# Optimization experiments

Hardware: AMD Instinct MI355X
Metric: run time of the kernel (lower is better)

## Reference

```python
import jax, jax.numpy as jnp
import numpy as np


def _gru_cell(x, h, W_ih, W_hh, b_ih, b_hh):
    # torch.nn.GRUCell semantics, gate order (r, z, n)
    gi = x @ W_ih.T + b_ih          # [B, 3H]
    gh = h @ W_hh.T + b_hh          # [B, 3H]
    ir, iz, inn = jnp.split(gi, 3, axis=-1)
    hr, hz, hn = jnp.split(gh, 3, axis=-1)
    r = jax.nn.sigmoid(ir + hr)
    z = jax.nn.sigmoid(iz + hz)
    n = jnp.tanh(inn + r * hn)
    return (1.0 - z) * n + z * h


def setup_inputs() -> dict:
    key = jax.random.key(0)
    ks = jax.random.split(key, 9)
    B, T, X, H = 128, 512, 64, 256
    s = 0.05
    return {
        "input": jax.random.normal(ks[0], (B, T, X), jnp.float32),
        "h_enc": jax.random.normal(ks[1], (B, H), jnp.float32),
        "W_ih": jax.random.normal(ks[2], (3 * H, X), jnp.float32) * s,
        "W_hh": jax.random.normal(ks[3], (3 * H, H), jnp.float32) * s,
        "b_ih": jnp.zeros((3 * H,), jnp.float32),
        "b_hh": jnp.zeros((3 * H,), jnp.float32),
        "W_out": jax.random.normal(ks[4], (X, H), jnp.float32) * s,
        "b_out": jnp.zeros((X,), jnp.float32),
        "mask0": jax.random.randint(ks[5], (T,), 0, 2, jnp.int32),
        "mask1": jax.random.randint(ks[6], (T,), 0, 2, jnp.int32),
        "skip_size": 4,
    }


def _skip_tables(T, skip):
    # Replicates Python-list negative indexing of the original forward.
    # Skip-list position at the GRU call (pre-append):  2i   if i<skip else i-skip
    # Skip-list position at the projection (post-append): 2i+1 if i<skip else i-skip
    # Positions < skip are zero placeholders; position p >= skip is H[p-skip].
    g_idx = np.zeros(T, np.int32); g_zero = np.zeros(T, bool)
    p_idx = np.zeros(T, np.int32); p_zero = np.zeros(T, bool)
    for i in range(T):
        pg = 2 * i if i < skip else i - skip
        pp = 2 * i + 1 if i < skip else i - skip
        g_zero[i] = pg < skip; g_idx[i] = max(pg - skip, 0)
        p_zero[i] = pp < skip; p_idx[i] = max(pp - skip, 0)
    return g_idx, g_zero, p_idx, p_zero


def reference(input, h_enc, W_ih, W_hh, b_ih, b_hh, W_out, b_out, mask0, mask1, skip_size):
    B, T, X = input.shape
    H = h_enc.shape[1]
    g_idx, g_zero, p_idx, p_zero = _skip_tables(T, int(skip_size))
    m0 = mask0.astype(input.dtype)
    m1 = mask1.astype(input.dtype)

    xs = (jnp.arange(T), m0, m1,
          jnp.asarray(g_idx), jnp.asarray(g_zero),
          jnp.asarray(p_idx), jnp.asarray(p_zero))

    def step(carry, sx):
        h_prev, x_prev, buf = carry          # buf: [T, B, H] history of GRU outputs
        i, a0, a1, gi, gz, pi, pz = sx
        skip_g = jnp.where(gz, 0.0, buf[gi])            # [B, H]
        hidden = h_prev * a0 + skip_g * a1
        h_new = _gru_cell(x_prev, hidden, W_ih, W_hh, b_ih, b_hh)
        buf = buf.at[i].set(h_new)                       # append H[i]
        skip_p = jnp.where(pz, 0.0, buf[pi])
        out = (h_prev + skip_p) @ W_out.T + b_out        # [B, X]
        return (h_new, out, buf), out

    buf0 = jnp.zeros((T, B, H), input.dtype)
    go = jnp.zeros((B, X), input.dtype)                  # GO token
    (_, _, _), outs = jax.lax.scan(step, (h_enc, go, buf0), xs)
    return jnp.transpose(outs, (1, 0, 2))                # [B, T, X]
```

## Files before the change

kernel.cpp:

```cpp
#include <hip/hip_runtime.h>

typedef _Float16 h2_t __attribute__((ext_vector_type(2)));

constexpr int T_ = 512;
constexpr int X_ = 64;
constexpr int H_ = 256;
constexpr int NWG = 128;
constexpr int NT = 512;
constexpr int RS = 16;

constexpr int GHH_U4 = 3 * 2 * 16 * 256;
constexpr int GIH_U4 = 3 * 2 * 4 * 256;
constexpr int GOUT_U4 = 2048;
constexpr int G_TOTAL = GHH_U4 + GIH_U4 + GOUT_U4;

__device__ __forceinline__ float sigmoid_f(float x) {
  float e = __expf(fminf(-x, 80.f));
  return 1.f / (1.f + e);
}
__device__ __forceinline__ float tanh_f(float x) {
  float e = __expf(fminf(-2.f * x, 80.f));
  return (1.f - e) / (1.f + e);
}

__device__ __forceinline__ unsigned pk2(float a, float b) {
  h2_t v;
  v[0] = (_Float16)a;
  v[1] = (_Float16)b;
  return __builtin_bit_cast(unsigned, v);
}
__device__ __forceinline__ uint4 pk8(const float* s) {
  return make_uint4(pk2(s[0], s[1]), pk2(s[2], s[3]), pk2(s[4], s[5]),
                    pk2(s[6], s[7]));
}

__device__ __forceinline__ float dotp(unsigned w, unsigned h, float acc) {
  h2_t wv = __builtin_bit_cast(h2_t, w);
  h2_t hv = __builtin_bit_cast(h2_t, h);
#if __has_builtin(__builtin_amdgcn_fdot2)
  return __builtin_amdgcn_fdot2(wv, hv, acc, false);
#else
  acc = fmaf((float)wv[0], (float)hv[0], acc);
  return fmaf((float)wv[1], (float)hv[1], acc);
#endif
}
__device__ __forceinline__ float dotq(uint4 w, uint4 h, float acc) {
  acc = dotp(w.x, h.x, acc);
  acc = dotp(w.y, h.y, acc);
  acc = dotp(w.z, h.z, acc);
  acc = dotp(w.w, h.w, acc);
  return acc;
}

__global__ void prep_kernel(const float* __restrict__ Wih,
                            const float* __restrict__ Whh,
                            const float* __restrict__ Wout,
                            uint4* __restrict__ G) {
  int id = blockIdx.x * 256 + threadIdx.x;
  if (id < GHH_U4) {
    int c = id & 255, r = id >> 8;
    int j = r & 15, gk = r >> 4, g = gk >> 1, kh = gk & 1;
    G[id] = pk8(Whh + (size_t)(g * 256 + c) * H_ + kh * 128 + j * 8);
  } else if (id < GHH_U4 + GIH_U4) {
    int jd = id - GHH_U4;
    int c = jd & 255, r = jd >> 8;
    int j = r & 3, gk = r >> 2, g = gk >> 1, kh = gk & 1;
    G[id] = pk8(Wih + (size_t)(g * 256 + c) * X_ + kh * 32 + j * 8);
  } else if (id < G_TOTAL) {
    int jd = id - GHH_U4 - GIH_U4;
    int u = jd >> 9, tt = jd & 511;
    int xcp = tt >> 3, sl = tt & 7;
    G[id] = pk8(Wout + (size_t)xcp * H_ + sl * 32 + u * 8);
  }
}

#define PTW(cp) (((cp) >> 4) * 36 + ((cp)&15))

#define PIN4(V4)                                                             \
  asm volatile("" : "+v"((V4).x), "+v"((V4).y), "+v"((V4).z), "+v"((V4).w))


#define GATES(p, i, hn)                                                      \
  float hn;                                                                  \
  {                                                                          \
    float a0 = 0, a1 = 0, z0 = 0, z1 = 0, n0 = 0, n1 = 0, ni = 0;            \
    const uint4* h4 = ((const uint4*)hid2[p]) + kh * 16;                     \
    _Pragma("unroll") for (int j = 0; j < 16; j += 2) {                      \
      uint4 ha = h4[j], hb = h4[j + 1];                                      \
      a0 = dotq(whh[j], ha, a0);                                             \
      a1 = dotq(whh[j + 1], hb, a1);                                         \
      z0 = dotq(whh[16 + j], ha, z0);                                        \
      z1 = dotq(whh[17 + j], hb, z1);                                        \
      n0 = dotq(whh[32 + j], ha, n0);                                        \
      n1 = dotq(whh[33 + j], hb, n1);                                        \
    }                                                                        \
    const uint4* x4 = ((const uint4*)xt2[p]) + kh * 4;                       \
    _Pragma("unroll") for (int j = 0; j < 4; ++j) {                          \
      uint4 x8 = x4[j];                                                      \
      a0 = dotq(wlih[j * NT + t], x8, a0);                                   \
      z0 = dotq(wlih[(4 + j) * NT + t], x8, z0);                             \
      ni = dotq(wlih[(8 + j) * NT + t], x8, ni);                             \
    }                                                                        \
    float ar = a0 + a1, az = z0 + z1, anh = n0 + n1;                         \
    ar += __shfl_xor(ar, 1);                                                 \
    az += __shfl_xor(az, 1);                                                 \
    anh += __shfl_xor(anh, 1);                                               \
    ni += __shfl_xor(ni, 1);                                                 \
    float r = sigmoid_f(ar + bsr);                                           \
    float z = sigmoid_f(az + bsz);                                           \
    float n = tanh_f(ni + bin_ + r * (anh + bhn_));                          \
    hn = fmaf(z, hid_reg - n, n);                    \
    if (kh == 0) ring[(i) & (RS - 1)][c] = hn;                               \
  }

#define PROJ(p, q, i)                                                        \
  {                                                                          \
    float fa = 0;                                                            \
    const uint4* p4 = (const uint4*)&pt2[p][sl * 36];                        \
    _Pragma("unroll") for (int j = 0; j < 4; ++j) fa =                       \
        dotq(wout_r[j * NT + t], p4[j], fa);                                 \
    fa += __shfl_xor(fa, 1);                                                 \
    fa += __shfl_xor(fa, 2);                                                 \
    fa += __shfl_xor(fa, 4);                                                 \
    float o = fa + bo;                                                       \
    if (sl == 0) out[ob + (size_t)(i)*X_ + xc] = o;                          \
    float oo = __shfl_xor(o, 8);                                             \
    if ((t & 15) == 0) xt2[q][t >> 4] = pk2(o, oo);                          \
  }

#define MSTEP(i, p, q)                                                       \
  {                                                                          \
    GATES(p, i, hn)                                                          \
    __builtin_amdgcn_sched_barrier(0);                                       \
    PROJ(p, q, i)                                                            \
    __builtin_amdgcn_sched_barrier(0);                                       \
    if ((i) + 1 < T_) {                                                      \
      float sgp = ring[((i) + 1 - 2 * skip) & (RS - 1)][c];                  \
      float hidn = m0f[(i) + 1] * hn + m1f[(i) + 1] * sgp;                   \
      float ptn = hn + sgp;                                                  \
      hid_reg = hidn;                                                        \
      float ho = __shfl_xor(hidn, 2);                                        \
      float po = __shfl_xor(ptn, 2);                                         \
      if ((t & 3) == 0) {                                                    \
        hid2[q][t >> 2] = pk2(hidn, ho);                                     \
        pt2[q][PTW(t >> 2)] = pk2(ptn, po);                                  \
      }                                                                      \
    }                                                                        \
    __syncthreads();                                                         \
  }

__global__ __launch_bounds__(NT, 1) void decoder_kernel(
    const float* __restrict__ h_enc, const float* __restrict__ b_ih,
    const float* __restrict__ b_hh, const float* __restrict__ b_out,
    const int* __restrict__ mask0, const int* __restrict__ mask1,
    const int* __restrict__ skipp, const uint4* __restrict__ G,
    float* __restrict__ out) {
  __shared__ alignas(16) uint4 wlih[12 * NT];
  __shared__ alignas(16) uint4 wout_r[4 * NT];
  __shared__ float ring[RS][H_];
  __shared__ alignas(16) unsigned hid2[2][H_ / 2];
  __shared__ alignas(16) unsigned pt2[2][8 * 36];
  __shared__ alignas(16) unsigned xt2[2][X_ / 2];
  __shared__ float m0f[T_], m1f[T_];

  const int t = threadIdx.x;
  const int b = blockIdx.x;
  const int c = t >> 1, kh = t & 1;
  const int xc = t >> 3, sl = t & 7;
  const size_t ob = (size_t)b * T_ * X_;

  uint4 whh[48];
#pragma unroll
  for (int u = 0; u < 48; ++u)
    whh[u] = G[((u >> 4) * 32 + kh * 16 + (u & 15)) * 256 + c];
#pragma unroll
  for (int u = 0; u < 48; ++u) PIN4(whh[u]);

#pragma unroll
  for (int u = 0; u < 12; ++u)
    wlih[u * NT + t] = G[GHH_U4 + ((u >> 2) * 8 + kh * 4 + (u & 3)) * 256 + c];
#pragma unroll
  for (int j = 0; j < 4; ++j)
    wout_r[j * NT + t] = G[GHH_U4 + GIH_U4 + j * NT + t];
  m0f[t] = (float)mask0[t];
  m1f[t] = (float)mask1[t];

  const int skip = skipp[0];
  const int i0 = (skip == 0) ? T_ : ((2 * skip < T_) ? 2 * skip : T_);

  const float bsr = b_ih[c] + b_hh[c];
  const float bsz = b_ih[H_ + c] + b_hh[H_ + c];
  const float bin_ = b_ih[2 * H_ + c];
  const float bhn_ = b_hh[2 * H_ + c];
  const float bo = b_out[xc];

  float hp = h_enc[(size_t)b * H_ + c];
  float hid_reg = (float)mask0[0] * hp;
  float hps_reg = hp;
  {
    float ho = __shfl_xor(hid_reg, 2);
    if ((t & 3) == 0) hid2[0][t >> 2] = pk2(hid_reg, ho);
  }
  if (t < X_ / 2) xt2[0][t] = 0u;
  __syncthreads();

  for (int i = 0; i < i0; ++i) {
    const int p = i & 1, q = p ^ 1;
    GATES(p, i, hn)
    {
      int ppos = (i < skip) ? 2 * i + 1 : i - skip;
      bool pz = ppos < skip;
      int pi = ppos - skip;
      if (pi < 0) pi = 0;
      float sp = pz ? 0.f : ((pi == i) ? hn : ring[pi & (RS - 1)][c]);
      float ptv = hps_reg + sp;
      float po = __shfl_xor(ptv, 2);
      if ((t & 3) == 0) pt2[p][PTW(t >> 2)] = pk2(ptv, po);
    }
    if (i + 1 < T_) {
      int i1 = i + 1;
      int pg = (i1 < skip) ? 2 * i1 : i1 - skip;
      bool gz = pg < skip;
      int gi = pg - skip;
      if (gi < 0) gi = 0;
      if (gi >= i1) gz = true;
      float sg = gz ? 0.f : ((gi == i) ? hn : ring[gi & (RS - 1)][c]);
      float hidn = m0f[i1] * hn + m1f[i1] * sg;
      hid_reg = hidn;
      float ho = __shfl_xor(hidn, 2);
      if ((t & 3) == 0) hid2[q][t >> 2] = pk2(hidn, ho);
      if (skip > 0 && i1 >= 2 * skip) {
        float sgp = ring[(i1 - 2 * skip) & (RS - 1)][c];
        float ptn = hn + sgp;
        float po2 = __shfl_xor(ptn, 2);
        if ((t & 3) == 0) pt2[q][PTW(t >> 2)] = pk2(ptn, po2);
      }
    }
    hps_reg = hn;
    __syncthreads();
    PROJ(p, q, i)
    __syncthreads();
  }

#pragma unroll 1
  for (int i = i0; i < T_; i += 2) {
    MSTEP(i, 0, 1)
    MSTEP(i + 1, 1, 0)
  }
}

extern "C" void kernel_launch(void* const* d_in, const int* in_sizes, int n_in,
                              void* d_out, int out_size, void* d_ws,
                              size_t ws_size, hipStream_t stream) {
  (void)in_sizes; (void)n_in; (void)out_size; (void)ws_size;
  const float* h_enc = (const float*)d_in[1];
  const float* W_ih = (const float*)d_in[2];
  const float* W_hh = (const float*)d_in[3];
  const float* b_ih = (const float*)d_in[4];
  const float* b_hh = (const float*)d_in[5];
  const float* W_out = (const float*)d_in[6];
  const float* b_out = (const float*)d_in[7];
  const int* mask0 = (const int*)d_in[8];
  const int* mask1 = (const int*)d_in[9];
  const int* skipp = (const int*)d_in[10];
  float* out = (float*)d_out;
  uint4* G = (uint4*)d_ws;

  prep_kernel<<<dim3(G_TOTAL / 256), dim3(256), 0, stream>>>(W_ih, W_hh,
                                                             W_out, G);
  decoder_kernel<<<dim3(NWG), dim3(NT), 0, stream>>>(
      h_enc, b_ih, b_hh, b_out, mask0, mask1, skipp, G, out);
}
```

Baseline: 1.131 ms.

## Rebalance weight residency between registers and LDS with contiguous prep layout

Moves W_ih and W_out weights from shared memory into registers and moves the n-gate W_hh slice from registers into shared memory. The prep kernel now writes weights in a per-thread contiguous layout so that each load is a simple strided index. The launch attributes change from launch_bounds(NT,1) to an explicit waves_per_eu(2,2), and the asm register pinning is removed. The goal is to balance VGPR and LDS use for the recurrent loop, at the cost of extra LDS reads for the n-gate weights on every step.

Result: faster. 1.054 ms (-6.8%).

```diff
diff --git a/kernel.cpp b/kernel.cpp
--- a/kernel.cpp
+++ b/kernel.cpp
@@ -9,10 +9,7 @@
 constexpr int NT = 512;
 constexpr int RS = 16;
 
-constexpr int GHH_U4 = 3 * 2 * 16 * 256;
-constexpr int GIH_U4 = 3 * 2 * 4 * 256;
-constexpr int GOUT_U4 = 2048;
-constexpr int G_TOTAL = GHH_U4 + GIH_U4 + GOUT_U4;
+constexpr int G_TOTAL = 64 * NT;
 
 __device__ __forceinline__ float sigmoid_f(float x) {
   float e = __expf(fminf(-x, 80.f));
@@ -57,27 +54,25 @@
                             const float* __restrict__ Wout,
                             uint4* __restrict__ G) {
   int id = blockIdx.x * 256 + threadIdx.x;
-  if (id < GHH_U4) {
-    int c = id & 255, r = id >> 8;
-    int j = r & 15, gk = r >> 4, g = gk >> 1, kh = gk & 1;
+  if (id >= G_TOTAL) return;
+  int t = id & (NT - 1), u = id >> 9;
+  int c = t >> 1, kh = t & 1;
+  if (u < 32) {
+    int g = u >> 4, j = u & 15;
     G[id] = pk8(Whh + (size_t)(g * 256 + c) * H_ + kh * 128 + j * 8);
-  } else if (id < GHH_U4 + GIH_U4) {
-    int jd = id - GHH_U4;
-    int c = jd & 255, r = jd >> 8;
-    int j = r & 3, gk = r >> 2, g = gk >> 1, kh = gk & 1;
+  } else if (u < 48) {
+    int j = u - 32;
+    G[id] = pk8(Whh + (size_t)(512 + c) * H_ + kh * 128 + j * 8);
+  } else if (u < 60) {
+    int v = u - 48, g = v >> 2, j = v & 3;
     G[id] = pk8(Wih + (size_t)(g * 256 + c) * X_ + kh * 32 + j * 8);
-  } else if (id < G_TOTAL) {
-    int jd = id - GHH_U4 - GIH_U4;
-    int u = jd >> 9, tt = jd & 511;
-    int xcp = tt >> 3, sl = tt & 7;
-    G[id] = pk8(Wout + (size_t)xcp * H_ + sl * 32 + u * 8);
+  } else {
+    int j = u - 60, xc = t >> 3, sl = t & 7;
+    G[id] = pk8(Wout + (size_t)xc * H_ + sl * 32 + j * 8);
   }
 }
 
 #define PTW(cp) (((cp) >> 4) * 36 + ((cp)&15))
-
-#define PIN4(V4)                                                             \
-  asm volatile("" : "+v"((V4).x), "+v"((V4).y), "+v"((V4).z), "+v"((V4).w))
 
 
 #define GATES(p, i, hn)                                                      \
@@ -86,20 +81,21 @@
     float a0 = 0, a1 = 0, z0 = 0, z1 = 0, n0 = 0, n1 = 0, ni = 0;            \
     const uint4* h4 = ((const uint4*)hid2[p]) + kh * 16;                     \
     _Pragma("unroll") for (int j = 0; j < 16; j += 2) {                      \
-      uint4 ha = h4[j], hb = h4[j + 1];                                      \
-      a0 = dotq(whh[j], ha, a0);                                             \
-      a1 = dotq(whh[j + 1], hb, a1);                                         \
-      z0 = dotq(whh[16 + j], ha, z0);                                        \
-      z1 = dotq(whh[17 + j], hb, z1);                                        \
-      n0 = dotq(whh[32 + j], ha, n0);                                        \
-      n1 = dotq(whh[33 + j], hb, n1);                                        \
+      uint4 ha = h4[j], hb = h4[j + 1];          \
+      uint4 wna = wn4[j * NT + t], wnb = wn4[(j + 1) * NT + t];              \
+      a0 = dotq(whh_rz[j], ha, a0);                                          \
+      a1 = dotq(whh_rz[j + 1], hb, a1);                                      \
+      z0 = dotq(whh_rz[16 + j], ha, z0);                                     \
+      z1 = dotq(whh_rz[17 + j], hb, z1);                                     \
+      n0 = dotq(wna, ha, n0);                                                \
+      n1 = dotq(wnb, hb, n1);                                                \
     }                                                                        \
     const uint4* x4 = ((const uint4*)xt2[p]) + kh * 4;                       \
     _Pragma("unroll") for (int j = 0; j < 4; ++j) {                          \
-      uint4 x8 = x4[j];                                                      \
-      a0 = dotq(wlih[j * NT + t], x8, a0);                                   \
-      z0 = dotq(wlih[(4 + j) * NT + t], x8, z0);                             \
-      ni = dotq(wlih[(8 + j) * NT + t], x8, ni);                             \
+      uint4 xa = x4[j];                                                      \
+      a0 = dotq(wih[j], xa, a0);                                             \
+      z0 = dotq(wih[4 + j], xa, z0);                                         \
+      ni = dotq(wih[8 + j], xa, ni);                                         \
     }                                                                        \
     float ar = a0 + a1, az = z0 + z1, anh = n0 + n1;                         \
     ar += __shfl_xor(ar, 1);                                                 \
@@ -118,7 +114,7 @@
     float fa = 0;                                                            \
     const uint4* p4 = (const uint4*)&pt2[p][sl * 36];                        \
     _Pragma("unroll") for (int j = 0; j < 4; ++j) fa =                       \
-        dotq(wout_r[j * NT + t], p4[j], fa);                                 \
+        dotq(wout[j], p4[j], fa);                                            \
     fa += __shfl_xor(fa, 1);                                                 \
     fa += __shfl_xor(fa, 2);                                                 \
     fa += __shfl_xor(fa, 4);                                                 \
@@ -149,14 +145,14 @@
     __syncthreads();                                                         \
   }
 
-__global__ __launch_bounds__(NT, 1) void decoder_kernel(
+__global__ __attribute__((amdgpu_flat_work_group_size(NT, NT),
+                          amdgpu_waves_per_eu(2, 2))) void decoder_kernel(
     const float* __restrict__ h_enc, const float* __restrict__ b_ih,
     const float* __restrict__ b_hh, const float* __restrict__ b_out,
     const int* __restrict__ mask0, const int* __restrict__ mask1,
     const int* __restrict__ skipp, const uint4* __restrict__ G,
     float* __restrict__ out) {
-  __shared__ alignas(16) uint4 wlih[12 * NT];
-  __shared__ alignas(16) uint4 wout_r[4 * NT];
+  __shared__ alignas(16) uint4 wn4[16 * NT];
   __shared__ float ring[RS][H_];
   __shared__ alignas(16) unsigned hid2[2][H_ / 2];
   __shared__ alignas(16) unsigned pt2[2][8 * 36];
@@ -169,19 +165,18 @@
   const int xc = t >> 3, sl = t & 7;
   const size_t ob = (size_t)b * T_ * X_;
 
-  uint4 whh[48];
-#pragma unroll
-  for (int u = 0; u < 48; ++u)
-    whh[u] = G[((u >> 4) * 32 + kh * 16 + (u & 15)) * 256 + c];
-#pragma unroll
-  for (int u = 0; u < 48; ++u) PIN4(whh[u]);
-
-#pragma unroll
-  for (int u = 0; u < 12; ++u)
-    wlih[u * NT + t] = G[GHH_U4 + ((u >> 2) * 8 + kh * 4 + (u & 3)) * 256 + c];
-#pragma unroll
-  for (int j = 0; j < 4; ++j)
-    wout_r[j * NT + t] = G[GHH_U4 + GIH_U4 + j * NT + t];
+  uint4 whh_rz[32];
+  uint4 wih[12];
+  uint4 wout[4];
+#pragma unroll
+  for (int u = 0; u < 32; ++u) whh_rz[u] = G[u * NT + t];
+#pragma unroll
+  for (int u = 0; u < 12; ++u) wih[u] = G[(48 + u) * NT + t];
+#pragma unroll
+  for (int u = 0; u < 4; ++u) wout[u] = G[(60 + u) * NT + t];
+
+#pragma unroll
+  for (int u = 0; u < 16; ++u) wn4[u * NT + t] = G[(32 + u) * NT + t];
   m0f[t] = (float)mask0[t];
   m1f[t] = (float)mask1[t];
 
```
